# Optimization experiments

Measured on AMD Instinct MI355X. Metric: run time of the kernel, lower is better.

The kernel has to match this reference:

```python
import jax, jax.numpy as jnp
import numpy as np

N_CLUSTERS = 1024
EMBED_DIM = 256
BETA = 0.25
EPS = 1e-05


def setup_inputs() -> dict:
    key = jax.random.key(0)
    k1, k2 = jax.random.split(key)
    z = jax.random.normal(k1, (16, 64, 64, EMBED_DIM), dtype=jnp.float32)
    # nn.init.uniform_(codebook, -1/K, 1/K)
    bound = 1.0 / N_CLUSTERS
    codebook = jax.random.uniform(k2, (N_CLUSTERS, EMBED_DIM), dtype=jnp.float32,
                                  minval=-bound, maxval=bound)
    return {"z": z, "codebook": codebook}


def reference(z, codebook):
    K = codebook.shape[0]
    # squared distances: ||z||^2 + ||e||^2 - 2 z.e  -> [B,V,P,K]
    z2 = jnp.sum(z * z, axis=-1, keepdims=True)          # [B,V,P,1]
    e2 = jnp.sum(codebook * codebook, axis=-1)           # [K]
    ze = jnp.einsum('bvpd,kd->bvpk', z, codebook)        # [B,V,P,K]
    dist = z2 + e2[None, None, None, :] - 2.0 * ze
    indices = jnp.argmin(dist, axis=-1)                  # [B,V,P] int
    z_q = codebook[indices]                              # gather [B,V,P,D]
    z_q_st = z + jax.lax.stop_gradient(z_q - z)          # straight-through

    codebook_loss = jnp.mean((z_q - jax.lax.stop_gradient(z)) ** 2)
    commitment_loss = jnp.mean((z - jax.lax.stop_gradient(z_q)) ** 2)
    cluster_loss = codebook_loss + BETA * commitment_loss

    # perplexity stats (no grad)
    counts = jnp.zeros((K,), dtype=jnp.float32).at[indices.ravel()].add(1.0)
    probs = counts / (counts.sum() + EPS)
    perplexity = jnp.exp(-jnp.sum(probs * jnp.log(probs + EPS)))

    return z_q_st, commitment_loss, codebook_loss, cluster_loss, perplexity, indices
```

## Files before the change

### kernel.cpp

```cpp
#include <hip/hip_runtime.h>
#include <cfloat>
#include <math.h>

#define P_TOT 65536
#define DIM   256
#define KTOT  1024
#define BETA_ 0.25f
#define EPS_  1e-5f
#define MARGIN_ 1.5e-4f

#define OUT_LOSS_OFF ((size_t)P_TOT * DIM)
#define OUT_IDX_OFF  (OUT_LOSS_OFF + 4)

typedef __attribute__((ext_vector_type(8))) short s16x8;
typedef __attribute__((ext_vector_type(4))) float f32x4;

__device__ __forceinline__ unsigned short f2bf(float x) {
    unsigned u = __float_as_uint(x);
    u += 0x7FFFu + ((u >> 16) & 1u);
    return (unsigned short)(u >> 16);
}
__device__ __forceinline__ float bf2f(unsigned short h) {
    return __uint_as_float(((unsigned)h) << 16);
}
__device__ __forceinline__ void gl16(const void* g, void* l) {
    __builtin_amdgcn_global_load_lds(
        (const __attribute__((address_space(1))) unsigned int*)g,
        (__attribute__((address_space(3))) unsigned int*)l, 16, 0, 0);
}

__global__ __launch_bounds__(256) void vq_pre(
    const float* __restrict__ z, const float* __restrict__ cb,
    float* __restrict__ z2, float* __restrict__ e2,
    char* __restrict__ cbi, unsigned int* __restrict__ hist,
    float* __restrict__ loss_sum, unsigned int* __restrict__ flag_cnt,
    float* __restrict__ out)
{
    const int tid = threadIdx.x;
    const int lane = tid & 63;
    const int wave = tid >> 6;
    const int bid = blockIdx.x;

    if (bid < P_TOT / 4) {
        const int p = bid * 4 + wave;
        float4 v = *(const float4*)(z + (size_t)p * DIM + lane * 4);
        float s = v.x * v.x + v.y * v.y + v.z * v.z + v.w * v.w;
        #pragma unroll
        for (int off = 32; off > 0; off >>= 1) s += __shfl_down(s, off, 64);
        if (lane == 0) z2[p] = s;

        unsigned short h0 = f2bf(v.x), h1 = f2bf(v.y), h2 = f2bf(v.z), h3 = f2bf(v.w);
        unsigned short l0 = f2bf(v.x - bf2f(h0)), l1 = f2bf(v.y - bf2f(h1));
        unsigned short l2 = f2bf(v.z - bf2f(h2)), l3 = f2bf(v.w - bf2f(h3));
        uint2 hp, lp;
        hp.x = (unsigned)h0 | ((unsigned)h1 << 16); hp.y = (unsigned)h2 | ((unsigned)h3 << 16);
        lp.x = (unsigned)l0 | ((unsigned)l1 << 16); lp.y = (unsigned)l2 | ((unsigned)l3 << 16);
        char* rowb = (char*)out + (size_t)p * 1024;
        *(uint2*)(rowb + lane * 8) = hp;
        *(uint2*)(rowb + 512 + lane * 8) = lp;
    } else {
        const int rel = bid - P_TOT / 4;
        const int k = rel * 4 + wave;
        float4 v = *(const float4*)(cb + (size_t)k * DIM + lane * 4);
        float s = v.x * v.x + v.y * v.y + v.z * v.z + v.w * v.w;
        #pragma unroll
        for (int off = 32; off > 0; off >>= 1) s += __shfl_down(s, off, 64);
        if (lane == 0) e2[k] = s;

        unsigned short h0 = f2bf(v.x), h1 = f2bf(v.y), h2 = f2bf(v.z), h3 = f2bf(v.w);
        unsigned short l0 = f2bf(v.x - bf2f(h0)), l1 = f2bf(v.y - bf2f(h1));
        unsigned short l2 = f2bf(v.z - bf2f(h2)), l3 = f2bf(v.w - bf2f(h3));
        uint2 hp, lp;
        hp.x = (unsigned)h0 | ((unsigned)h1 << 16); hp.y = (unsigned)h2 | ((unsigned)h3 << 16);
        lp.x = (unsigned)l0 | ((unsigned)l1 << 16); lp.y = (unsigned)l2 | ((unsigned)l3 << 16);
        char* rowb = cbi + (size_t)k * 1024;
        *(uint2*)(rowb + lane * 8) = hp;
        *(uint2*)(rowb + 512 + lane * 8) = lp;

        if (rel < 4) hist[rel * 256 + tid] = 0u;
        if (rel == 4 && tid == 0) { *loss_sum = 0.0f; *flag_cnt = 0u; }
    }
}

#define BM 128
#define BN 128

__global__ __launch_bounds__(256, 2) void vq_argmin(
    const float* __restrict__ z, const float* __restrict__ cb,
    const char* __restrict__ cbi,
    const float* __restrict__ z2, const float* __restrict__ e2,
    unsigned int* __restrict__ hist, float* __restrict__ loss_sum,
    unsigned int* __restrict__ flag_cnt, unsigned int* __restrict__ flag_list,
    float* __restrict__ out)
{
    __shared__ __align__(16) char sm[32768];
    __shared__ float sb1[BM][2];
    __shared__ float sb2[BM][2];
    __shared__ int   si1[BM][2];
    __shared__ int kwin[BM];
    __shared__ unsigned char flgs[BM];
    __shared__ float wred[4];

    const int tid = threadIdx.x;
    const int lane = tid & 63;
    const int wid = tid >> 6;
    const int wm = wid >> 1, wn = wid & 1;
    const int col = lane & 15;
    const int lg  = lane >> 4;
    const int row0 = blockIdx.x * BM;

    const char* zsB = (const char*)out;

    float b1[16], b2[16]; int i1[16];
    float z2r[16];
    #pragma unroll
    for (int q = 0; q < 16; ++q) {
        b1[q] = FLT_MAX; b2[q] = FLT_MAX; i1[q] = 0;
        z2r[q] = z2[row0 + wm * 64 + (q >> 2) * 16 + lg * 4 + (q & 3)];
    }

    int aOff[4], bOff[4];
    #pragma unroll
    for (int f = 0; f < 4; ++f) {
        const int pbl = (lg ^ (col & 7)) << 4;
        aOff[f] = (wm * 64 + f * 16 + col) * 128 + pbl;
        bOff[f] = (wn * 64 + f * 16 + col) * 128 + pbl;
    }

    const int sr = lane >> 3;
    const int pb = lane & 7;
    const int lb = pb ^ sr;
    const int srcColBase = ((lb & 4) << 7) + ((lb & 3) << 4);

    #pragma unroll 1
    for (int nc = 0; nc < KTOT / BN; ++nc) {
        const int n0 = nc * BN;
        f32x4 acc[4][4];
        #pragma unroll
        for (int fm = 0; fm < 4; ++fm)
            #pragma unroll
            for (int fn = 0; fn < 4; ++fn)
                acc[fm][fn] = (f32x4){0.0f, 0.0f, 0.0f, 0.0f};

        #pragma unroll 1
        for (int k8 = 0; k8 < 8; ++k8) {
            __syncthreads();
            const int srcCol = k8 * 64 + srcColBase;
            const size_t brow0 = ((size_t)(nc << 7)) << 10;
            #pragma unroll
            for (int i = 0; i < 4; ++i) {
                const int rb = i * 32 + wid * 8;
                const int r = rb + sr;
                char* ldst = sm + rb * 128;
                gl16(zsB + (((size_t)(row0 + r)) << 10) + srcCol, ldst);
                gl16(cbi + brow0 + (((size_t)r) << 10) + srcCol, ldst + 16384);
            }
            __syncthreads();
            s16x8 ah[4], al[4], bh[4], bl[4];
            #pragma unroll
            for (int f = 0; f < 4; ++f) {
                ah[f] = *(const s16x8*)(sm + aOff[f]);
                al[f] = *(const s16x8*)(sm + (aOff[f] ^ 64));
                bh[f] = *(const s16x8*)(sm + 16384 + bOff[f]);
                bl[f] = *(const s16x8*)(sm + 16384 + (bOff[f] ^ 64));
            }
            #pragma unroll
            for (int fm = 0; fm < 4; ++fm)
                #pragma unroll
                for (int fn = 0; fn < 4; ++fn) {
                    acc[fm][fn] = __builtin_amdgcn_mfma_f32_16x16x32_bf16(
                        ah[fm], bh[fn], acc[fm][fn], 0, 0, 0);
                    acc[fm][fn] = __builtin_amdgcn_mfma_f32_16x16x32_bf16(
                        ah[fm], bl[fn], acc[fm][fn], 0, 0, 0);
                    acc[fm][fn] = __builtin_amdgcn_mfma_f32_16x16x32_bf16(
                        al[fm], bh[fn], acc[fm][fn], 0, 0, 0);
                }
        }
        const float* ep = e2 + n0 + wn * 64 + col;
        const float e2v[4] = {ep[0], ep[16], ep[32], ep[48]};
        #pragma unroll
        for (int fm = 0; fm < 4; ++fm)
            #pragma unroll
            for (int fn = 0; fn < 4; ++fn)
                #pragma unroll
                for (int r4 = 0; r4 < 4; ++r4) {
                    const int q = fm * 4 + r4;
                    const float dist = (z2r[q] + e2v[fn]) - 2.0f * acc[fm][fn][r4];
                    const int idx = n0 + wn * 64 + fn * 16 + col;
                    if (dist < b1[q]) { b2[q] = b1[q]; b1[q] = dist; i1[q] = idx; }
                    else if (dist < b2[q]) { b2[q] = dist; }
                }
    }

    #pragma unroll
    for (int q = 0; q < 16; ++q) {
        float x1 = b1[q], x2 = b2[q]; int xi = i1[q];
        #pragma unroll
        for (int m = 1; m < 16; m <<= 1) {
            const float y1 = __shfl_xor(x1, m, 64);
            const float y2 = __shfl_xor(x2, m, 64);
            const int   yi = __shfl_xor(xi, m, 64);
            const float nb2 = fminf(fmaxf(x1, y1), fminf(x2, y2));
            if (y1 < x1 || (y1 == x1 && yi < xi)) { x1 = y1; xi = yi; }
            x2 = nb2;
        }
        if (col == 0) {
            const int px = wm * 64 + (q >> 2) * 16 + lg * 4 + (q & 3);
            sb1[px][wn] = x1; sb2[px][wn] = x2; si1[px][wn] = xi;
        }
    }
    __syncthreads();
    if (tid < BM) {
        float x1 = sb1[tid][0], x2 = sb2[tid][0]; int xi = si1[tid][0];
        const float y1 = sb1[tid][1], y2 = sb2[tid][1]; const int yi = si1[tid][1];
        const float nb2 = fminf(fmaxf(x1, y1), fminf(x2, y2));
        if (y1 < x1 || (y1 == x1 && yi < xi)) { x1 = y1; xi = yi; }
        x2 = nb2;
        kwin[tid] = xi;
        const bool fl = (x2 - x1) <= MARGIN_;
        flgs[tid] = fl ? 1 : 0;
        if (fl) {
            const unsigned pos = atomicAdd(flag_cnt, 1u);
            flag_list[pos] = (unsigned)(row0 + tid);
        } else {
            out[OUT_IDX_OFF + row0 + tid] = (float)xi;
            atomicAdd(&hist[xi], 1u);
        }
    }
    __syncthreads();

    float lacc = 0.0f;
    #pragma unroll 4
    for (int i = 0; i < 32; ++i) {
        const int flat4 = tid + i * 256;
        const int row = flat4 >> 6;
        if (!flgs[row]) {
            const int dj = (flat4 & 63) * 4;
            const size_t zoff = (size_t)(row0 + row) * DIM + dj;
            float4 zv = *(const float4*)(z + zoff);
            float4 ev = *(const float4*)(cb + (size_t)kwin[row] * DIM + dj);
            float dx = ev.x - zv.x, dy = ev.y - zv.y, dz = ev.z - zv.z, dw = ev.w - zv.w;
            float4 o;
            o.x = zv.x + dx; o.y = zv.y + dy; o.z = zv.z + dz; o.w = zv.w + dw;
            *(float4*)(out + zoff) = o;
            lacc += dx * dx + dy * dy + dz * dz + dw * dw;
        }
    }
    #pragma unroll
    for (int off = 32; off > 0; off >>= 1) lacc += __shfl_down(lacc, off, 64);
    if (lane == 0) wred[wid] = lacc;
    __syncthreads();
    if (tid == 0) atomicAdd(loss_sum, wred[0] + wred[1] + wred[2] + wred[3]);
}

__global__ __launch_bounds__(256) void vq_fix(
    const float* __restrict__ z, const float* __restrict__ cb,
    const float* __restrict__ z2, const float* __restrict__ e2,
    const unsigned int* __restrict__ flag_cnt, const unsigned int* __restrict__ flag_list,
    unsigned int* __restrict__ hist, float* __restrict__ loss_sum,
    float* __restrict__ out)
{
    __shared__ float zrow[4][DIM];
    __shared__ float zz2[4];
    __shared__ int pxid[4];
    __shared__ float rb[4][256];
    __shared__ int   ri[4][256];
    __shared__ int   kw4[4];

    const int tid = threadIdx.x;
    const int total = (int)*flag_cnt;

    for (int base = blockIdx.x * 4; base < total; base += gridDim.x * 4) {
        const int npx = min(4, total - base);
        __syncthreads();
        if (tid < 4) {
            const int p = (int)flag_list[base + (tid < npx ? tid : 0)];
            pxid[tid] = p; zz2[tid] = z2[p];
        }
        __syncthreads();
        {
            const int q = tid >> 6, d = (tid & 63) * 4;
            float4 v = *(const float4*)(z + (size_t)pxid[q] * DIM + d);
            *(float4*)&zrow[q][d] = v;
        }
        __syncthreads();

        const int k0 = tid * 4;
        float acc[4][4];
        #pragma unroll
        for (int q = 0; q < 4; ++q)
            #pragma unroll
            for (int j = 0; j < 4; ++j) acc[q][j] = 0.0f;

        for (int d4 = 0; d4 < 64; ++d4) {
            float4 cv[4];
            #pragma unroll
            for (int j = 0; j < 4; ++j)
                cv[j] = *(const float4*)(cb + (size_t)(k0 + j) * DIM + d4 * 4);
            #pragma unroll
            for (int q = 0; q < 4; ++q) {
                float4 zv = *(const float4*)&zrow[q][d4 * 4];
                #pragma unroll
                for (int j = 0; j < 4; ++j) {
                    acc[q][j] = fmaf(zv.x, cv[j].x, acc[q][j]);
                    acc[q][j] = fmaf(zv.y, cv[j].y, acc[q][j]);
                    acc[q][j] = fmaf(zv.z, cv[j].z, acc[q][j]);
                    acc[q][j] = fmaf(zv.w, cv[j].w, acc[q][j]);
                }
            }
        }
        #pragma unroll
        for (int q = 0; q < 4; ++q) {
            float bd = FLT_MAX; int bi = 0;
            #pragma unroll
            for (int j = 0; j < 4; ++j) {
                const int k = k0 + j;
                const float dist = (zz2[q] + e2[k]) - 2.0f * acc[q][j];
                if (dist < bd) { bd = dist; bi = k; }
            }
            rb[q][tid] = bd; ri[q][tid] = bi;
        }
        __syncthreads();
        {
            const int q = tid >> 6, lane = tid & 63;
            float bd = rb[q][lane]; int bi = ri[q][lane];
            #pragma unroll
            for (int s = 1; s < 4; ++s) {
                const float d2 = rb[q][lane + s * 64]; const int i2 = ri[q][lane + s * 64];
                if (d2 < bd || (d2 == bd && i2 < bi)) { bd = d2; bi = i2; }
            }
            #pragma unroll
            for (int off = 32; off > 0; off >>= 1) {
                const float d2 = __shfl_down(bd, off, 64);
                const int i2 = __shfl_down(bi, off, 64);
                if (d2 < bd || (d2 == bd && i2 < bi)) { bd = d2; bi = i2; }
            }
            if (lane == 0) kw4[q] = bi;
        }
        __syncthreads();
        {
            const int q = tid >> 6, lane = tid & 63;
            if (q < npx) {
                const int p = pxid[q];
                const int kw = kw4[q];
                const int d = lane * 4;
                float4 zv = *(const float4*)&zrow[q][d];
                float4 ev = *(const float4*)(cb + (size_t)kw * DIM + d);
                float dx = ev.x - zv.x, dy = ev.y - zv.y, dz = ev.z - zv.z, dw = ev.w - zv.w;
                float4 o;
                o.x = zv.x + dx; o.y = zv.y + dy; o.z = zv.z + dz; o.w = zv.w + dw;
                *(float4*)(out + (size_t)p * DIM + d) = o;
                float lacc = dx * dx + dy * dy + dz * dz + dw * dw;
                #pragma unroll
                for (int off = 32; off > 0; off >>= 1) lacc += __shfl_down(lacc, off, 64);
                if (lane == 0) {
                    atomicAdd(loss_sum, lacc);
                    out[OUT_IDX_OFF + p] = (float)kw;
                    atomicAdd(&hist[kw], 1u);
                }
            }
        }
    }
}

__global__ __launch_bounds__(1024) void vq_finalize(
    const unsigned int* __restrict__ hist, const float* __restrict__ loss_sum,
    float* __restrict__ out)
{
    __shared__ float sred[16];
    __shared__ float totalsh;
    const int tid = threadIdx.x;
    const float c = (float)hist[tid];

    float t = c;
    #pragma unroll
    for (int off = 32; off > 0; off >>= 1) t += __shfl_down(t, off, 64);
    if ((tid & 63) == 0) sred[tid >> 6] = t;
    __syncthreads();
    if (tid == 0) {
        float s = 0.0f;
        for (int i = 0; i < 16; ++i) s += sred[i];
        totalsh = s;
    }
    __syncthreads();
    const float total = totalsh;
    const float prob = c / (total + EPS_);
    float term = prob * logf(prob + EPS_);
    __syncthreads();
    #pragma unroll
    for (int off = 32; off > 0; off >>= 1) term += __shfl_down(term, off, 64);
    if ((tid & 63) == 0) sred[tid >> 6] = term;
    __syncthreads();
    if (tid == 0) {
        float s = 0.0f;
        for (int i = 0; i < 16; ++i) s += sred[i];
        const float perp = expf(-s);
        const float S = *loss_sum;
        const float mean = S / (float)(P_TOT * DIM);
        out[OUT_LOSS_OFF + 0] = mean;
        out[OUT_LOSS_OFF + 1] = mean;
        out[OUT_LOSS_OFF + 2] = mean + BETA_ * mean;
        out[OUT_LOSS_OFF + 3] = perp;
    }
}

extern "C" void kernel_launch(void* const* d_in, const int* in_sizes, int n_in,
                              void* d_out, int out_size, void* d_ws, size_t ws_size,
                              hipStream_t stream) {
    const float* z  = (const float*)d_in[0];
    const float* cb = (const float*)d_in[1];
    float* out = (float*)d_out;

    float* z2 = (float*)d_ws;
    float* e2 = z2 + P_TOT;
    unsigned int* hist = (unsigned int*)(e2 + KTOT);
    float* loss_sum = (float*)(hist + KTOT);
    unsigned int* flag_cnt = (unsigned int*)(loss_sum + 1);
    unsigned int* flag_list = flag_cnt + 1;
    char* cbi = (char*)(((uintptr_t)(flag_list + P_TOT) + 15) & ~(uintptr_t)15);

    vq_pre<<<P_TOT / 4 + KTOT / 4, 256, 0, stream>>>(z, cb, z2, e2, cbi, hist,
                                                     loss_sum, flag_cnt, out);
    vq_argmin<<<P_TOT / BM, 256, 0, stream>>>(z, cb, cbi, z2, e2,
                                              hist, loss_sum, flag_cnt, flag_list, out);
    vq_fix<<<1024, 256, 0, stream>>>(z, cb, z2, e2, flag_cnt, flag_list,
                                     hist, loss_sum, out);
    vq_finalize<<<1, 1024, 0, stream>>>(hist, loss_sum, out);
}
```

Baseline: 412.1 us.

## Use 512-thread blocks with 8 waves splitting N and deeper K stages

The argmin GEMM kernel moves from 4 waves (2x2, each 64x64) to 8 waves (2x4, each 64x32) per 128x128 tile. Each K stage now loads twice as much data (two 64-byte sub-slices into a 64KB LDS buffer), which halves the number of barrier-separated stages. Candidate reduction goes through LDS across 4 N-waves. The intent is more waves to hide latency and fewer syncs, at the cost of less register reuse per wave, higher LDS use and one block per CU.

```diff
diff --git a/kernel.cpp b/kernel.cpp
--- a/kernel.cpp
+++ b/kernel.cpp
@@ -85,7 +85,7 @@
 #define BM 128
 #define BN 128
 
-__global__ __launch_bounds__(256, 2) void vq_argmin(
+__global__ __launch_bounds__(512, 1) void vq_argmin(
     const float* __restrict__ z, const float* __restrict__ cb,
     const char* __restrict__ cbi,
     const float* __restrict__ z2, const float* __restrict__ e2,
@@ -93,18 +93,16 @@
     unsigned int* __restrict__ flag_cnt, unsigned int* __restrict__ flag_list,
     float* __restrict__ out)
 {
-    __shared__ __align__(16) char sm[32768];
-    __shared__ float sb1[BM][2];
-    __shared__ float sb2[BM][2];
-    __shared__ int   si1[BM][2];
+    __shared__ __align__(16) char sm[65536];
     __shared__ int kwin[BM];
     __shared__ unsigned char flgs[BM];
-    __shared__ float wred[4];
+    __shared__ float wred[8];
 
     const int tid = threadIdx.x;
     const int lane = tid & 63;
     const int wid = tid >> 6;
-    const int wm = wid >> 1, wn = wid & 1;
+    const int wm = wid >> 2;
+    const int wn = wid & 3;
     const int col = lane & 15;
     const int lg  = lane >> 4;
     const int row0 = blockIdx.x * BM;
@@ -119,13 +117,13 @@
         z2r[q] = z2[row0 + wm * 64 + (q >> 2) * 16 + lg * 4 + (q & 3)];
     }
 
-    int aOff[4], bOff[4];
-    #pragma unroll
-    for (int f = 0; f < 4; ++f) {
-        const int pbl = (lg ^ (col & 7)) << 4;
-        aOff[f] = (wm * 64 + f * 16 + col) * 128 + pbl;
-        bOff[f] = (wn * 64 + f * 16 + col) * 128 + pbl;
-    }
+    int aOff[4], bOff[2];
+    #pragma unroll
+    for (int f = 0; f < 4; ++f)
+        aOff[f] = (wm * 64 + f * 16 + col) * 128 + ((lg ^ (col & 7)) << 4);
+    #pragma unroll
+    for (int f = 0; f < 2; ++f)
+        bOff[f] = (wn * 32 + f * 16 + col) * 128 + ((lg ^ (col & 7)) << 4);
 
     const int sr = lane >> 3;
     const int pb = lane & 7;
@@ -135,63 +133,78 @@
     #pragma unroll 1
     for (int nc = 0; nc < KTOT / BN; ++nc) {
         const int n0 = nc * BN;
-        f32x4 acc[4][4];
+        const size_t brow0 = ((size_t)(nc << 7)) << 10;
+        f32x4 acc[4][2];
         #pragma unroll
         for (int fm = 0; fm < 4; ++fm)
             #pragma unroll
-            for (int fn = 0; fn < 4; ++fn)
+            for (int fn = 0; fn < 2; ++fn)
                 acc[fm][fn] = (f32x4){0.0f, 0.0f, 0.0f, 0.0f};
 
         #pragma unroll 1
-        for (int k8 = 0; k8 < 8; ++k8) {
+        for (int k8 = 0; k8 < 4; ++k8) {
             __syncthreads();
-            const int srcCol = k8 * 64 + srcColBase;
-            const size_t brow0 = ((size_t)(nc << 7)) << 10;
-            #pragma unroll
-            for (int i = 0; i < 4; ++i) {
-                const int rb = i * 32 + wid * 8;
-                const int r = rb + sr;
-                char* ldst = sm + rb * 128;
-                gl16(zsB + (((size_t)(row0 + r)) << 10) + srcCol, ldst);
-                gl16(cbi + brow0 + (((size_t)r) << 10) + srcCol, ldst + 16384);
+            const int colb = k8 * 128 + srcColBase;
+            #pragma unroll
+            for (int ks = 0; ks < 2; ++ks) {
+                const int srcCol = colb + ks * 64;
+                #pragma unroll
+                for (int i = 0; i < 2; ++i) {
+                    const int slab = wid * 2 + i;
+                    const int r = slab * 8 + sr;
+                    char* la = sm + ks * 16384 + slab * 1024;
+                    gl16(zsB + (((size_t)(row0 + r)) << 10) + srcCol, la);
+                    gl16(cbi + brow0 + (((size_t)r) << 10) + srcCol, la + 32768);
+                }
             }
             __syncthreads();
-            s16x8 ah[4], al[4], bh[4], bl[4];
-            #pragma unroll
-            for (int f = 0; f < 4; ++f) {
-                ah[f] = *(const s16x8*)(sm + aOff[f]);
-                al[f] = *(const s16x8*)(sm + (aOff[f] ^ 64));
-                bh[f] = *(const s16x8*)(sm + 16384 + bOff[f]);
-                bl[f] = *(const s16x8*)(sm + 16384 + (bOff[f] ^ 64));
-            }
-            #pragma unroll
-            for (int fm = 0; fm < 4; ++fm)
-                #pragma unroll
-                for (int fn = 0; fn < 4; ++fn) {
-                    acc[fm][fn] = __builtin_amdgcn_mfma_f32_16x16x32_bf16(
-                        ah[fm], bh[fn], acc[fm][fn], 0, 0, 0);
-                    acc[fm][fn] = __builtin_amdgcn_mfma_f32_16x16x32_bf16(
-                        ah[fm], bl[fn], acc[fm][fn], 0, 0, 0);
-                    acc[fm][fn] = __builtin_amdgcn_mfma_f32_16x16x32_bf16(
-                        al[fm], bh[fn], acc[fm][fn], 0, 0, 0);
-                }
-        }
-        const float* ep = e2 + n0 + wn * 64 + col;
-        const float e2v[4] = {ep[0], ep[16], ep[32], ep[48]};
+            #pragma unroll
+            for (int ks = 0; ks < 2; ++ks) {
+                const char* at = sm + ks * 16384;
+                s16x8 ah[4], al[4], bh[2], bl[2];
+                #pragma unroll
+                for (int f = 0; f < 4; ++f) {
+                    ah[f] = *(const s16x8*)(at + aOff[f]);
+                    al[f] = *(const s16x8*)(at + (aOff[f] ^ 64));
+                }
+                #pragma unroll
+                for (int f = 0; f < 2; ++f) {
+                    bh[f] = *(const s16x8*)(at + 32768 + bOff[f]);
+                    bl[f] = *(const s16x8*)(at + 32768 + (bOff[f] ^ 64));
+                }
+                #pragma unroll
+                for (int fm = 0; fm < 4; ++fm)
+                    #pragma unroll
+                    for (int fn = 0; fn < 2; ++fn) {
+                        acc[fm][fn] = __builtin_amdgcn_mfma_f32_16x16x32_bf16(
+                            ah[fm], bh[fn], acc[fm][fn], 0, 0, 0);
+                        acc[fm][fn] = __builtin_amdgcn_mfma_f32_16x16x32_bf16(
+                            ah[fm], bl[fn], acc[fm][fn], 0, 0, 0);
+                        acc[fm][fn] = __builtin_amdgcn_mfma_f32_16x16x32_bf16(
+                            al[fm], bh[fn], acc[fm][fn], 0, 0, 0);
+                    }
+            }
+        }
+        const float* ep = e2 + n0 + wn * 32 + col;
+        const float e2v[2] = {ep[0], ep[16]};
         #pragma unroll
         for (int fm = 0; fm < 4; ++fm)
             #pragma unroll
-            for (int fn = 0; fn < 4; ++fn)
+            for (int fn = 0; fn < 2; ++fn)
                 #pragma unroll
                 for (int r4 = 0; r4 < 4; ++r4) {
                     const int q = fm * 4 + r4;
                     const float dist = (z2r[q] + e2v[fn]) - 2.0f * acc[fm][fn][r4];
-                    const int idx = n0 + wn * 64 + fn * 16 + col;
+                    const int idx = n0 + wn * 32 + fn * 16 + col;
                     if (dist < b1[q]) { b2[q] = b1[q]; b1[q] = dist; i1[q] = idx; }
                     else if (dist < b2[q]) { b2[q] = dist; }
                 }
     }
 
+    __syncthreads();
+    float* Rb1 = (float*)sm;
+    float* Rb2 = (float*)(sm + 2048);
+    int*   Ri1 = (int*)(sm + 4096);
     #pragma unroll
     for (int q = 0; q < 16; ++q) {
         float x1 = b1[q], x2 = b2[q]; int xi = i1[q];
@@ -206,16 +219,20 @@
         }
         if (col == 0) {
             const int px = wm * 64 + (q >> 2) * 16 + lg * 4 + (q & 3);
-            sb1[px][wn] = x1; sb2[px][wn] = x2; si1[px][wn] = xi;
+            Rb1[px * 4 + wn] = x1; Rb2[px * 4 + wn] = x2; Ri1[px * 4 + wn] = xi;
         }
     }
     __syncthreads();
     if (tid < BM) {
-        float x1 = sb1[tid][0], x2 = sb2[tid][0]; int xi = si1[tid][0];
-        const float y1 = sb1[tid][1], y2 = sb2[tid][1]; const int yi = si1[tid][1];
-        const float nb2 = fminf(fmaxf(x1, y1), fminf(x2, y2));
-        if (y1 < x1 || (y1 == x1 && yi < xi)) { x1 = y1; xi = yi; }
-        x2 = nb2;
+        float x1 = Rb1[tid * 4], x2 = Rb2[tid * 4]; int xi = Ri1[tid * 4];
+        #pragma unroll
+        for (int s = 1; s < 4; ++s) {
+            const float c1 = Rb1[tid * 4 + s], c2 = Rb2[tid * 4 + s];
+            const int ci = Ri1[tid * 4 + s];
+            const float nb2 = fminf(fmaxf(x1, c1), fminf(x2, c2));
+            if (c1 < x1 || (c1 == x1 && ci < xi)) { x1 = c1; xi = ci; }
+            x2 = nb2;
+        }
         kwin[tid] = xi;
         const bool fl = (x2 - x1) <= MARGIN_;
         flgs[tid] = fl ? 1 : 0;
@@ -231,8 +248,8 @@
 
     float lacc = 0.0f;
     #pragma unroll 4
-    for (int i = 0; i < 32; ++i) {
-        const int flat4 = tid + i * 256;
+    for (int i = 0; i < 16; ++i) {
+        const int flat4 = tid + i * 512;
         const int row = flat4 >> 6;
         if (!flgs[row]) {
             const int dj = (flat4 & 63) * 4;
@@ -250,7 +267,12 @@
     for (int off = 32; off > 0; off >>= 1) lacc += __shfl_down(lacc, off, 64);
     if (lane == 0) wred[wid] = lacc;
     __syncthreads();
-    if (tid == 0) atomicAdd(loss_sum, wred[0] + wred[1] + wred[2] + wred[3]);
+    if (tid == 0) {
+        float s = 0.0f;
+        #pragma unroll
+        for (int w = 0; w < 8; ++w) s += wred[w];
+        atomicAdd(loss_sum, s);
+    }
 }
 
 __global__ __launch_bounds__(256) void vq_fix(
@@ -421,7 +443,7 @@
 
     vq_pre<<<P_TOT / 4 + KTOT / 4, 256, 0, stream>>>(z, cb, z2, e2, cbi, hist,
                                                      loss_sum, flag_cnt, out);
-    vq_argmin<<<P_TOT / BM, 256, 0, stream>>>(z, cb, cbi, z2, e2,
+    vq_argmin<<<P_TOT / BM, 512, 0, stream>>>(z, cb, cbi, z2, e2,
                                               hist, loss_sum, flag_cnt, flag_list, out);
     vq_fix<<<1024, 256, 0, stream>>>(z, cb, z2, e2, flag_cnt, flag_list,
                                      hist, loss_sum, out);
```

New measurement: 453.3 us. 1.1x slower.

## Double-buffer LDS tiles to overlap global loads with MFMA compute

Applied to the files above, without the earlier changes.

Flattens the codebook-chunk and K-slice loops into one 64-step loop and double-buffers the shared-memory tiles, issuing the next step's global-to-LDS loads before computing on the current buffer. This removes one barrier per step and is meant to hide load latency behind the bf16 MFMA work. Shared memory grows from 32 KB to 64 KB per block, which may limit the two-blocks-per-CU occupancy the launch bounds ask for.

```diff
diff --git a/kernel.cpp b/kernel.cpp
--- a/kernel.cpp
+++ b/kernel.cpp
@@ -93,7 +93,7 @@
     unsigned int* __restrict__ flag_cnt, unsigned int* __restrict__ flag_list,
     float* __restrict__ out)
 {
-    __shared__ __align__(16) char sm[32768];
+    __shared__ __align__(16) char sm[65536];
     __shared__ float sb1[BM][2];
     __shared__ float sb2[BM][2];
     __shared__ int   si1[BM][2];
@@ -128,68 +128,88 @@
     }
 
     const int sr = lane >> 3;
-    const int pb = lane & 7;
-    const int lb = pb ^ sr;
+    const int lb = (lane & 7) ^ sr;
     const int srcColBase = ((lb & 4) << 7) + ((lb & 3) << 4);
 
+    size_t aRowB[4], bRowB[4];
+    int ldsD[4];
+    #pragma unroll
+    for (int i = 0; i < 4; ++i) {
+        const int rb = i * 32 + wid * 8;
+        ldsD[i]  = rb * 128;
+        aRowB[i] = ((size_t)(row0 + rb + sr)) << 10;
+        bRowB[i] = ((size_t)(rb + sr)) << 10;
+    }
+
+    #pragma unroll
+    for (int i = 0; i < 4; ++i) {
+        gl16(zsB + aRowB[i] + srcColBase, sm + ldsD[i]);
+        gl16(cbi + bRowB[i] + srcColBase, sm + 16384 + ldsD[i]);
+    }
+    __syncthreads();
+
+    f32x4 acc[4][4];
+
     #pragma unroll 1
-    for (int nc = 0; nc < KTOT / BN; ++nc) {
-        const int n0 = nc * BN;
-        f32x4 acc[4][4];
-        #pragma unroll
-        for (int fm = 0; fm < 4; ++fm)
-            #pragma unroll
-            for (int fn = 0; fn < 4; ++fn)
-                acc[fm][fn] = (f32x4){0.0f, 0.0f, 0.0f, 0.0f};
-
-        #pragma unroll 1
-        for (int k8 = 0; k8 < 8; ++k8) {
-            __syncthreads();
-            const int srcCol = k8 * 64 + srcColBase;
-            const size_t brow0 = ((size_t)(nc << 7)) << 10;
-            #pragma unroll
-            for (int i = 0; i < 4; ++i) {
-                const int rb = i * 32 + wid * 8;
-                const int r = rb + sr;
-                char* ldst = sm + rb * 128;
-                gl16(zsB + (((size_t)(row0 + r)) << 10) + srcCol, ldst);
-                gl16(cbi + brow0 + (((size_t)r) << 10) + srcCol, ldst + 16384);
-            }
-            __syncthreads();
-            s16x8 ah[4], al[4], bh[4], bl[4];
-            #pragma unroll
-            for (int f = 0; f < 4; ++f) {
-                ah[f] = *(const s16x8*)(sm + aOff[f]);
-                al[f] = *(const s16x8*)(sm + (aOff[f] ^ 64));
-                bh[f] = *(const s16x8*)(sm + 16384 + bOff[f]);
-                bl[f] = *(const s16x8*)(sm + 16384 + (bOff[f] ^ 64));
-            }
+    for (int t = 0; t < 64; ++t) {
+        const int buf = t & 1;
+        if ((t & 7) == 0) {
             #pragma unroll
             for (int fm = 0; fm < 4; ++fm)
                 #pragma unroll
-                for (int fn = 0; fn < 4; ++fn) {
-                    acc[fm][fn] = __builtin_amdgcn_mfma_f32_16x16x32_bf16(
-                        ah[fm], bh[fn], acc[fm][fn], 0, 0, 0);
-                    acc[fm][fn] = __builtin_amdgcn_mfma_f32_16x16x32_bf16(
-                        ah[fm], bl[fn], acc[fm][fn], 0, 0, 0);
-                    acc[fm][fn] = __builtin_amdgcn_mfma_f32_16x16x32_bf16(
-                        al[fm], bh[fn], acc[fm][fn], 0, 0, 0);
-                }
-        }
-        const float* ep = e2 + n0 + wn * 64 + col;
-        const float e2v[4] = {ep[0], ep[16], ep[32], ep[48]};
+                for (int fn = 0; fn < 4; ++fn)
+                    acc[fm][fn] = (f32x4){0.0f, 0.0f, 0.0f, 0.0f};
+        }
+        if (t < 63) {
+            const int tn = t + 1;
+            const int srcCol = ((tn & 7) << 6) + srcColBase;
+            const size_t bnc = ((size_t)(tn >> 3)) << 17;
+            char* dst = sm + ((tn & 1) << 15);
+            #pragma unroll
+            for (int i = 0; i < 4; ++i) {
+                gl16(zsB + aRowB[i] + srcCol, dst + ldsD[i]);
+                gl16(cbi + bnc + bRowB[i] + srcCol, dst + 16384 + ldsD[i]);
+            }
+        }
+        const char* at = sm + (buf << 15);
+        s16x8 ah[4], al[4], bh[4], bl[4];
+        #pragma unroll
+        for (int f = 0; f < 4; ++f) {
+            ah[f] = *(const s16x8*)(at + aOff[f]);
+            al[f] = *(const s16x8*)(at + (aOff[f] ^ 64));
+            bh[f] = *(const s16x8*)(at + 16384 + bOff[f]);
+            bl[f] = *(const s16x8*)(at + 16384 + (bOff[f] ^ 64));
+        }
         #pragma unroll
         for (int fm = 0; fm < 4; ++fm)
             #pragma unroll
-            for (int fn = 0; fn < 4; ++fn)
+            for (int fn = 0; fn < 4; ++fn) {
+                acc[fm][fn] = __builtin_amdgcn_mfma_f32_16x16x32_bf16(
+                    ah[fm], bh[fn], acc[fm][fn], 0, 0, 0);
+                acc[fm][fn] = __builtin_amdgcn_mfma_f32_16x16x32_bf16(
+                    ah[fm], bl[fn], acc[fm][fn], 0, 0, 0);
+                acc[fm][fn] = __builtin_amdgcn_mfma_f32_16x16x32_bf16(
+                    al[fm], bh[fn], acc[fm][fn], 0, 0, 0);
+            }
+
+        if ((t & 7) == 7) {
+            const int n0 = (t >> 3) << 7;
+            const float* ep = e2 + n0 + wn * 64 + col;
+            const float e2v[4] = {ep[0], ep[16], ep[32], ep[48]};
+            #pragma unroll
+            for (int fm = 0; fm < 4; ++fm)
                 #pragma unroll
-                for (int r4 = 0; r4 < 4; ++r4) {
-                    const int q = fm * 4 + r4;
-                    const float dist = (z2r[q] + e2v[fn]) - 2.0f * acc[fm][fn][r4];
-                    const int idx = n0 + wn * 64 + fn * 16 + col;
-                    if (dist < b1[q]) { b2[q] = b1[q]; b1[q] = dist; i1[q] = idx; }
-                    else if (dist < b2[q]) { b2[q] = dist; }
-                }
+                for (int fn = 0; fn < 4; ++fn)
+                    #pragma unroll
+                    for (int r4 = 0; r4 < 4; ++r4) {
+                        const int q = fm * 4 + r4;
+                        const float dist = (z2r[q] + e2v[fn]) - 2.0f * acc[fm][fn][r4];
+                        const int idx = n0 + wn * 64 + fn * 16 + col;
+                        if (dist < b1[q]) { b2[q] = b1[q]; b1[q] = dist; i1[q] = idx; }
+                        else if (dist < b2[q]) { b2[q] = dist; }
+                    }
+        }
+        __syncthreads();
     }
 
     #pragma unroll
```

Measured after the change: 427.4 us. 1.04x slower.
